# Kernel optimization log

Hardware: AMD Instinct MI355X
Metric: run time of the kernel (lower is better)

## Reference

```python
import jax, jax.numpy as jnp
import numpy as np

B, S, DIM, COV = 64, 512, 1024, 256


def setup_inputs() -> dict:
    key = jax.random.key(0)
    ks = jax.random.split(key, 12)
    s = 0.02
    h = jax.random.normal(ks[0], (B, DIM), jnp.float32)
    context = jax.random.normal(ks[1], (B, S, DIM), jnp.float32)
    cov = jax.random.normal(ks[2], (B, S, COV), jnp.float32)
    mask = jax.random.randint(ks[3], (B, S), 0, 2) == 1
    W_in = jax.random.normal(ks[4], (DIM, DIM), jnp.float32) * s
    W_out = jax.random.normal(ks[5], (DIM, 2 * DIM), jnp.float32) * s
    W_cov = jax.random.normal(ks[6], (DIM, COV), jnp.float32) * s
    b_cov = jax.random.normal(ks[7], (DIM,), jnp.float32) * s
    w_ih = jax.random.normal(ks[8], (3 * COV, 2 * DIM + 1), jnp.float32) * s
    w_hh = jax.random.normal(ks[9], (3 * COV, COV), jnp.float32) * s
    b_ih = jax.random.normal(ks[10], (3 * COV,), jnp.float32) * s
    b_hh = jax.random.normal(ks[11], (3 * COV,), jnp.float32) * s
    return dict(h=h, context=context, cov=cov, W_in=W_in, W_out=W_out,
                W_cov=W_cov, b_cov=b_cov, w_ih=w_ih, w_hh=w_hh,
                b_ih=b_ih, b_hh=b_hh, mask=mask)


def reference(h, context, cov, W_in, W_out, W_cov, b_cov, w_ih, w_hh, b_ih, b_hh, mask):
    # coverage-adjusted context: context + cov_linear(cov)  [B,S,DIM]
    ctx = context + jnp.einsum('bsc,dc->bsd', cov, W_cov) + b_cov
    # target = linear_in(h)  [B,DIM]
    target = h @ W_in.T
    # scores = bmm(context, target).squeeze(2)  [B,S]
    attn = jnp.einsum('bsd,bd->bs', ctx, target)
    attn = jnp.where(mask, -jnp.inf, attn)
    attn = jax.nn.softmax(attn, axis=1)
    # weighted_context = bmm(attn3, context)  [B,DIM]
    wc = jnp.einsum('bs,bsd->bd', attn, ctx)
    h_tilde = jnp.tanh(jnp.concatenate([wc, h], axis=1) @ W_out.T)
    # single-step GRU coverage update over B*S rows
    h_exp = jnp.broadcast_to(h[:, None, :], (B, S, DIM))
    x = jnp.concatenate([ctx, h_exp, attn[..., None]], axis=-1).reshape(B * S, 2 * DIM + 1)
    h0 = cov.reshape(B * S, COV)
    gx = x @ w_ih.T + b_ih   # [B*S, 3*COV]
    gh = h0 @ w_hh.T + b_hh  # [B*S, 3*COV]
    xr, xz, xn = jnp.split(gx, 3, axis=1)
    hr, hz, hn = jnp.split(gh, 3, axis=1)
    r = jax.nn.sigmoid(xr + hr)
    z = jax.nn.sigmoid(xz + hz)
    n = jnp.tanh(xn + r * hn)
    new_cov = ((1.0 - z) * n + z * h0).reshape(B, S, COV)
    return h_tilde, attn, new_cov
```

## Files before the change

### kernel.cpp

```cpp
#include <hip/hip_runtime.h>
#include <math.h>

typedef unsigned short ushort_t;
typedef __attribute__((ext_vector_type(8))) short short8;
typedef __attribute__((ext_vector_type(4))) float f32x4;
typedef __attribute__((ext_vector_type(4))) unsigned short ushort4v;

constexpr int B_ = 64, S_ = 512, DIM_ = 1024, COV_ = 256, TC_ = 768, KIH_ = 2049;
constexpr int NG_ = 1024, KG_ = 1280;

__device__ __forceinline__ float b2f(ushort_t u) {
    union { unsigned int i; float f; } v; v.i = ((unsigned int)u) << 16; return v.f;
}
__device__ __forceinline__ ushort_t f2b(float f) {
    unsigned int x = __float_as_uint(f);
    unsigned int r = x + 0x7fffu + ((x >> 16) & 1u);
    return (ushort_t)(r >> 16);
}
__device__ __forceinline__ float ldv(const float* p, size_t i) { return p[i]; }
__device__ __forceinline__ float ldv(const ushort_t* p, size_t i) { return b2f(p[i]); }

__device__ __forceinline__ float wave_reduce(float a) {
#pragma unroll
    for (int off = 32; off >= 1; off >>= 1) a += __shfl_down(a, off, 64);
    return a;
}

__device__ __forceinline__ void xpose4(f32x4& v, int l) {
    float s, r;
    s = (l & 1) ? v[0] : v[1]; r = __shfl_xor(s, 1, 64); if (l & 1) v[0] = r; else v[1] = r;
    s = (l & 1) ? v[2] : v[3]; r = __shfl_xor(s, 1, 64); if (l & 1) v[2] = r; else v[3] = r;
    s = (l & 2) ? v[0] : v[2]; r = __shfl_xor(s, 2, 64); if (l & 2) v[0] = r; else v[2] = r;
    s = (l & 2) ? v[1] : v[3]; r = __shfl_xor(s, 2, 64); if (l & 2) v[1] = r; else v[3] = r;
}

#define GLDS16(src, dst)                                                            \
    __builtin_amdgcn_global_load_lds(                                               \
        (const __attribute__((address_space(1))) void*)(src),                       \
        (__attribute__((address_space(3))) void*)(dst), 16, 0, 0)

__global__ __launch_bounds__(256) void k_detect_p(const unsigned char* __restrict__ mask,
                                                  const ushort_t* __restrict__ win,
                                                  int* __restrict__ parts) {
    __shared__ int r0[256];
    __shared__ int r1[256];
    int bid = blockIdx.x, tid = threadIdx.x, mb = 0, f32 = 0;
    for (int i = bid * 256 + tid; i < 32768; i += 64 * 256)
        if ((i & 3) != 0 && mask[i] != 0) mb = 1;
    for (int i = bid * 256 + tid; i < 32768; i += 64 * 256) {
        ushort_t u = win[2 * i];
        if ((u & 0x7F80u) >= 0x4480u) f32 = 1;
    }
    r0[tid] = mb; r1[tid] = f32; __syncthreads();
    for (int st = 128; st >= 1; st >>= 1) {
        if (tid < st) { r0[tid] |= r0[tid + st]; r1[tid] |= r1[tid + st]; }
        __syncthreads();
    }
    if (tid == 0) { parts[bid] = r0[0]; parts[64 + bid] = r1[0]; }
}
__global__ void k_detect_c(const int* __restrict__ parts, int* __restrict__ flags) {
    int tid = threadIdx.x;
    int a = parts[tid], b = parts[64 + tid];
#pragma unroll
    for (int off = 32; off >= 1; off >>= 1) {
        a |= __shfl_down(a, off, 64);
        b |= __shfl_down(b, off, 64);
    }
    if (tid == 0) { flags[0] = a; flags[1] = b; }
}

template <typename IT>
__device__ __forceinline__ void transpose_body(const IT* __restrict__ in,
                                               ushort_t* __restrict__ out,
                                               int R, int C, int ld, int off) {
    int idx = blockIdx.x * 256 + threadIdx.x;
    if (idx >= R * C) return;
    int r = idx / C, c = idx - r * C;
    out[c * R + r] = f2b(ldv(in, (size_t)r * ld + off + c));
}
__global__ void k_transpose(const void* __restrict__ in, ushort_t* __restrict__ out,
                            int R, int C, int ld, int off, const int* __restrict__ flags) {
    if (flags[1]) transpose_body((const float*)in, out, R, C, ld, off);
    else transpose_body((const ushort_t*)in, out, R, C, ld, off);
}

template <typename IT>
__device__ __forceinline__ void bfold_body(const IT* __restrict__ bcov,
                                           const IT* __restrict__ wih,
                                           float* __restrict__ bfold,
                                           float* __restrict__ watt) {
    int j = blockIdx.x * 4 + (threadIdx.x >> 6);
    int lane = threadIdx.x & 63;
    const IT* wr = wih + (size_t)j * KIH_;
    float a = 0.f;
#pragma unroll
    for (int i = 0; i < 16; ++i) { int k = lane + 64 * i; a += ldv(bcov, k) * ldv(wr, k); }
    a = wave_reduce(a);
    if (lane == 0) { bfold[j] = a; watt[j] = ldv(wr, 2048); }
}
__global__ __launch_bounds__(256) void k_bfold(const void* __restrict__ bcov,
                                               const void* __restrict__ wih,
                                               float* __restrict__ bfold,
                                               float* __restrict__ watt,
                                               const int* __restrict__ flags) {
    if (flags[1]) bfold_body((const float*)bcov, (const float*)wih, bfold, watt);
    else bfold_body((const ushort_t*)bcov, (const ushort_t*)wih, bfold, watt);
}

__global__ __launch_bounds__(256) void k_wfold_p(const ushort_t* __restrict__ wcov_t,
                                                 const ushort_t* __restrict__ w_t,
                                                 float* __restrict__ wfp) {
    __shared__ float col[256];
    int c = blockIdx.x, p = blockIdx.y, tid = threadIdx.x;
    col[tid] = b2f(wcov_t[c * DIM_ + p * 256 + tid]);
    __syncthreads();
    float a0 = 0.f, a1 = 0.f, a2 = 0.f;
    const ushort_t* wt = w_t + (size_t)(p * 256) * TC_;
    for (int d = 0; d < 256; ++d) {
        float x = col[d];
        const ushort_t* wr = wt + d * TC_;
        a0 += x * b2f(wr[tid]);
        a1 += x * b2f(wr[tid + 256]);
        a2 += x * b2f(wr[tid + 512]);
    }
    float* o = wfp + ((size_t)p * COV_ + c) * TC_;
    o[tid] = a0;
    o[tid + 256] = a1;
    o[tid + 512] = a2;
}

__global__ __launch_bounds__(256) void k_wfold(const ushort_t* __restrict__ wcov_t,
                                               const ushort_t* __restrict__ w_t,
                                               float* __restrict__ wfold) {
    __shared__ float col[DIM_];
    int c = blockIdx.x, tid = threadIdx.x;
    for (int d = tid; d < DIM_; d += 256) col[d] = b2f(wcov_t[c * DIM_ + d]);
    __syncthreads();
    float a0 = 0.f, a1 = 0.f, a2 = 0.f;
    for (int d = 0; d < DIM_; ++d) {
        float x = col[d];
        const ushort_t* wr = w_t + d * TC_;
        a0 += x * b2f(wr[tid]);
        a1 += x * b2f(wr[tid + 256]);
        a2 += x * b2f(wr[tid + 512]);
    }
    wfold[c * TC_ + tid] = a0;
    wfold[c * TC_ + tid + 256] = a1;
    wfold[c * TC_ + tid + 512] = a2;
}

template <typename IT>
__device__ __forceinline__ void buildwg_body(const IT* __restrict__ wih,
                                             const IT* __restrict__ whh,
                                             const float* __restrict__ wfp,
                                             ushort_t* __restrict__ wg) {
    int idx = blockIdx.x * 256 + threadIdx.x;
    if (idx >= NG_ * KG_) return;
    int n = idx / KG_, k = idx - n * KG_;
    int g = n & 3, cq = n >> 2;
    int j = g * COV_ + cq;
    float v;
    if (k < DIM_) {
        v = (j < TC_) ? ldv(wih, (size_t)j * KIH_ + k) : 0.f;
    } else {
        int c = k - DIM_;
        float wf = 0.f;
        if (j < TC_) {
            size_t base = (size_t)c * TC_ + j;
            wf = wfp[base] + wfp[(size_t)COV_ * TC_ + base] +
                 wfp[2 * (size_t)COV_ * TC_ + base] + wfp[3 * (size_t)COV_ * TC_ + base];
        }
        if (j < 512)      v = wf + ldv(whh, (size_t)j * COV_ + c);
        else if (j < TC_) v = wf;
        else              v = ldv(whh, (size_t)(j - 256) * COV_ + c);
    }
    wg[(size_t)n * KG_ + k] = f2b(v);
}
__global__ void k_buildwg(const void* __restrict__ wih, const void* __restrict__ whh,
                          const float* __restrict__ wfp, ushort_t* __restrict__ wg,
                          const int* __restrict__ flags) {
    if (flags[1]) buildwg_body((const float*)wih, (const float*)whh, wfp, wg);
    else buildwg_body((const ushort_t*)wih, (const ushort_t*)whh, wfp, wg);
}

template <typename IT>
__device__ __forceinline__ void target_body(const IT* __restrict__ h,
                                            const IT* __restrict__ W_in,
                                            float* __restrict__ target) {
    int o = blockIdx.x * 4 + (threadIdx.x >> 6);
    int lane = threadIdx.x & 63;
    int b = o >> 10, d = o & (DIM_ - 1);
    const IT* hr = h + (size_t)b * DIM_;
    const IT* wr = W_in + (size_t)d * DIM_;
    float a = 0.f;
#pragma unroll
    for (int j = 0; j < 16; ++j) { int k = lane + 64 * j; a += ldv(hr, k) * ldv(wr, k); }
    a = wave_reduce(a);
    if (lane == 0) target[o] = a;
}
__global__ __launch_bounds__(256) void k_target_w(const void* __restrict__ h,
                                                  const void* __restrict__ W_in,
                                                  float* __restrict__ target,
                                                  const int* __restrict__ flags) {
    if (flags[1]) target_body((const float*)h, (const float*)W_in, target);
    else target_body((const ushort_t*)h, (const ushort_t*)W_in, target);
}

template <typename IT>
__device__ __forceinline__ void mvec_body(const float* __restrict__ target,
                                          const IT* __restrict__ W_cov,
                                          const IT* __restrict__ bcov,
                                          float* __restrict__ mvec,
                                          float* __restrict__ bct) {
    __shared__ float tg[DIM_];
    __shared__ float red[256];
    int b = blockIdx.x, q = blockIdx.y, tid = threadIdx.x;
    float pb = 0.f;
    for (int k = tid; k < DIM_; k += 256) {
        float t = target[b * DIM_ + k];
        tg[k] = t; pb += t * ldv(bcov, k);
    }
    red[tid] = pb; __syncthreads();
    for (int st = 128; st >= 1; st >>= 1) {
        if (tid < st) red[tid] += red[tid + st];
        __syncthreads();
    }
    if (q == 0 && tid == 0) bct[b] = red[0];
    __syncthreads();
    int cg = tid & 63, dg = tid >> 6;
    int c = q * 64 + cg;
    float acc = 0.f;
    int d0 = dg * 256;
    for (int d = d0; d < d0 + 256; ++d) acc += tg[d] * ldv(W_cov, (size_t)d * COV_ + c);
    red[dg * 64 + cg] = acc;
    __syncthreads();
    if (dg == 0)
        mvec[b * COV_ + c] = red[cg] + red[64 + cg] + red[128 + cg] + red[192 + cg];
}
__global__ __launch_bounds__(256) void k_mvec(const float* __restrict__ target,
                                              const void* __restrict__ W_cov,
                                              const void* __restrict__ bcov,
                                              float* __restrict__ mvec,
                                              float* __restrict__ bct,
                                              const int* __restrict__ flags) {
    if (flags[1]) mvec_body(target, (const float*)W_cov, (const float*)bcov, mvec, bct);
    else mvec_body(target, (const ushort_t*)W_cov, (const ushort_t*)bcov, mvec, bct);
}

template <typename IT>
__device__ __forceinline__ void scoreraw_body(const IT* __restrict__ context,
                                              const IT* __restrict__ cov,
                                              const float* __restrict__ target,
                                              const float* __restrict__ mvec,
                                              const float* __restrict__ bct,
                                              float* __restrict__ scf,
                                              ushort_t* __restrict__ ctx_bf,
                                              ushort_t* __restrict__ cov_bf) {
    __shared__ float tg[DIM_];
    __shared__ float ms[COV_];
    int b = blockIdx.x, tid = threadIdx.x;
    for (int k = tid; k < DIM_; k += 256) tg[k] = target[b * DIM_ + k];
    if (tid < COV_) ms[tid] = mvec[b * COV_ + tid];
    float bc = bct[b];
    __syncthreads();
    int wave = tid >> 6, lane = tid & 63;
    int s0 = blockIdx.y * 32 + wave * 8;
    for (int i = 0; i < 8; ++i) {
        int s = s0 + i;
        size_t row = (size_t)(b * S_ + s);
        const IT* cr = context + row * DIM_;
        const IT* vr = cov + row * COV_;
        float a = 0.f;
        if constexpr (sizeof(IT) == 4) {
#pragma unroll
            for (int j = 0; j < 4; ++j) {
                int d = lane * 4 + 256 * j;
                float4 x = *(const float4*)((const float*)cr + d);
                a += x.x * tg[d] + x.y * tg[d + 1] + x.z * tg[d + 2] + x.w * tg[d + 3];
                if (ctx_bf) {
                    ushort4v u;
                    u[0] = f2b(x.x); u[1] = f2b(x.y); u[2] = f2b(x.z); u[3] = f2b(x.w);
                    *(ushort4v*)(ctx_bf + row * DIM_ + d) = u;
                }
            }
            {
                int cc = lane * 4;
                float4 x = *(const float4*)((const float*)vr + cc);
                a += x.x * ms[cc] + x.y * ms[cc + 1] + x.z * ms[cc + 2] + x.w * ms[cc + 3];
                if (cov_bf) {
                    ushort4v u;
                    u[0] = f2b(x.x); u[1] = f2b(x.y); u[2] = f2b(x.z); u[3] = f2b(x.w);
                    *(ushort4v*)(cov_bf + row * COV_ + cc) = u;
                }
            }
        } else {
#pragma unroll
            for (int j = 0; j < 16; ++j) { int d = lane + 64 * j; a += ldv(cr, d) * tg[d]; }
#pragma unroll
            for (int j = 0; j < 4; ++j) { int c = lane + 64 * j; a += ldv(vr, c) * ms[c]; }
        }
        a = wave_reduce(a);
        if (lane == 0) scf[row] = a + bc;
    }
}
__global__ __launch_bounds__(256) void k_scoreraw(const void* __restrict__ context,
                                                  const void* __restrict__ cov,
                                                  const float* __restrict__ target,
                                                  const float* __restrict__ mvec,
                                                  const float* __restrict__ bct,
                                                  float* __restrict__ scf,
                                                  ushort_t* __restrict__ ctx_bf,
                                                  ushort_t* __restrict__ cov_bf,
                                                  const int* __restrict__ flags) {
    if (flags[1]) scoreraw_body((const float*)context, (const float*)cov, target, mvec, bct,
                                scf, ctx_bf, cov_bf);
    else scoreraw_body((const ushort_t*)context, (const ushort_t*)cov, target, mvec, bct,
                       scf, ctx_bf, cov_bf);
}

__global__ __launch_bounds__(256) void k_softmax(const float* __restrict__ scf,
                                                 const void* __restrict__ maskp,
                                                 const int* __restrict__ flags,
                                                 float* __restrict__ attnf,
                                                 float* __restrict__ attn_out) {
    __shared__ float red[256];
    int b = blockIdx.x, tid = threadIdx.x;
    int mb = flags[0];
    int i0 = b * S_ + tid, i1 = i0 + 256;
    int m0 = mb ? (int)((const unsigned char*)maskp)[i0] : ((const int*)maskp)[i0];
    int m1 = mb ? (int)((const unsigned char*)maskp)[i1] : ((const int*)maskp)[i1];
    float s0 = m0 ? -INFINITY : scf[i0];
    float s1 = m1 ? -INFINITY : scf[i1];
    red[tid] = fmaxf(s0, s1); __syncthreads();
    for (int st = 128; st >= 1; st >>= 1) {
        if (tid < st) red[tid] = fmaxf(red[tid], red[tid + st]);
        __syncthreads();
    }
    float mx = red[0]; __syncthreads();
    float e0 = expf(s0 - mx), e1 = expf(s1 - mx);
    red[tid] = e0 + e1; __syncthreads();
    for (int st = 128; st >= 1; st >>= 1) {
        if (tid < st) red[tid] += red[tid + st];
        __syncthreads();
    }
    float inv = 1.0f / red[0];
    float a0 = e0 * inv, a1 = e1 * inv;
    attnf[i0] = a0; attnf[i1] = a1;
    attn_out[i0] = a0; attn_out[i1] = a1;
}

__global__ __launch_bounds__(256) void k_wcpart2(const ushort_t* __restrict__ ctx_bf,
                                                 const ushort_t* __restrict__ cov_bf,
                                                 const void* __restrict__ ctx_in,
                                                 const void* __restrict__ cov_in,
                                                 const float* __restrict__ attnf,
                                                 float* __restrict__ wcp,
                                                 float* __restrict__ acp,
                                                 const int* __restrict__ flags) {
    const ushort_t* C = flags[1] ? ctx_bf : (const ushort_t*)ctx_in;
    const ushort_t* V = flags[1] ? cov_bf : (const ushort_t*)cov_in;
    __shared__ float at[32];
    int b = blockIdx.x, ch = blockIdx.y, tid = threadIdx.x;
    int s0 = ch * 32;
    if (tid < 32) at[tid] = attnf[b * S_ + s0 + tid];
    __syncthreads();
    float acv = 0.f;
    for (int s = 0; s < 32; ++s)
        acv += at[s] * b2f(V[((size_t)(b * S_ + s0 + s)) * COV_ + tid]);
    acp[((size_t)ch * B_ + b) * COV_ + tid] = acv;
    float acc[4] = {0.f, 0.f, 0.f, 0.f};
    for (int s = 0; s < 32; ++s) {
        float w = at[s];
        const ushort_t* cr = C + ((size_t)(b * S_ + s0 + s)) * DIM_;
        acc[0] += w * b2f(cr[tid]);
        acc[1] += w * b2f(cr[tid + 256]);
        acc[2] += w * b2f(cr[tid + 512]);
        acc[3] += w * b2f(cr[tid + 768]);
    }
    size_t base = ((size_t)ch * B_ + b) * DIM_;
    for (int m = 0; m < 4; ++m) wcp[base + tid + 256 * m] = acc[m];
}

template <typename IT>
__device__ __forceinline__ void wcfin_body(const float* __restrict__ wcp,
                                           const float* __restrict__ acp,
                                           const ushort_t* __restrict__ wcov_t,
                                           const IT* __restrict__ bcov,
                                           float* __restrict__ wc) {
    __shared__ float ac[COV_];
    int b = blockIdx.x, tid = threadIdx.x;
    float a = 0.f;
    for (int ch = 0; ch < 16; ++ch) a += acp[((size_t)ch * B_ + b) * COV_ + tid];
    ac[tid] = a;
    __syncthreads();
    float acc[4] = {0.f, 0.f, 0.f, 0.f};
    for (int ch = 0; ch < 16; ++ch) {
        size_t base = ((size_t)ch * B_ + b) * DIM_;
        for (int m = 0; m < 4; ++m) acc[m] += wcp[base + tid + 256 * m];
    }
    for (int c = 0; c < COV_; ++c) {
        float av = ac[c];
        const ushort_t* wr = wcov_t + c * DIM_;
        acc[0] += av * b2f(wr[tid]);
        acc[1] += av * b2f(wr[tid + 256]);
        acc[2] += av * b2f(wr[tid + 512]);
        acc[3] += av * b2f(wr[tid + 768]);
    }
    for (int m = 0; m < 4; ++m) {
        int d = tid + 256 * m;
        wc[b * DIM_ + d] = acc[m] + ldv(bcov, d);
    }
}
__global__ __launch_bounds__(256) void k_wcfin(const float* __restrict__ wcp,
                                               const float* __restrict__ acp,
                                               const ushort_t* __restrict__ wcov_t,
                                               const void* __restrict__ bcov,
                                               float* __restrict__ wc,
                                               const int* __restrict__ flags) {
    if (flags[1]) wcfin_body(wcp, acp, wcov_t, (const float*)bcov, wc);
    else wcfin_body(wcp, acp, wcov_t, (const ushort_t*)bcov, wc);
}

template <typename IT>
__device__ __forceinline__ void htilde_body(const float* __restrict__ wc,
                                            const IT* __restrict__ h,
                                            const IT* __restrict__ W_out,
                                            float* __restrict__ out_ht) {
    int o = blockIdx.x * 4 + (threadIdx.x >> 6);
    int lane = threadIdx.x & 63;
    int b = o >> 10, d = o & (DIM_ - 1);
    const float* wcr = wc + b * DIM_;
    const IT* hr = h + (size_t)b * DIM_;
    const IT* wr = W_out + (size_t)d * 2 * DIM_;
    float a = 0.f;
#pragma unroll
    for (int j = 0; j < 16; ++j) { int k = lane + 64 * j; a += wcr[k] * ldv(wr, k); }
#pragma unroll
    for (int j = 0; j < 16; ++j) { int k = lane + 64 * j; a += ldv(hr, k) * ldv(wr, DIM_ + k); }
    a = wave_reduce(a);
    if (lane == 0) out_ht[o] = tanhf(a);
}
__global__ __launch_bounds__(256) void k_htilde_w(const float* __restrict__ wc,
                                                  const void* __restrict__ h,
                                                  const void* __restrict__ W_out,
                                                  float* __restrict__ out_ht,
                                                  const int* __restrict__ flags) {
    if (flags[1]) htilde_body(wc, (const float*)h, (const float*)W_out, out_ht);
    else htilde_body(wc, (const ushort_t*)h, (const ushort_t*)W_out, out_ht);
}

template <typename IT>
__device__ __forceinline__ void gxh_body(const IT* __restrict__ h,
                                         const IT* __restrict__ w_ih,
                                         const IT* __restrict__ b_ih,
                                         const float* __restrict__ bfold,
                                         float* __restrict__ gxall) {
    int o = blockIdx.x * 4 + (threadIdx.x >> 6);
    int lane = threadIdx.x & 63;
    int b = o / TC_, j = o - b * TC_;
    const IT* hr = h + (size_t)b * DIM_;
    const IT* wr = w_ih + (size_t)j * KIH_ + DIM_;
    float a = 0.f;
#pragma unroll
    for (int i = 0; i < 16; ++i) { int k = lane + 64 * i; a += ldv(hr, k) * ldv(wr, k); }
    a = wave_reduce(a);
    if (lane == 0) gxall[o] = a + ldv(b_ih, j) + bfold[j];
}
__global__ __launch_bounds__(256) void k_gxh_w(const void* __restrict__ h,
                                               const void* __restrict__ w_ih,
                                               const void* __restrict__ b_ih,
                                               const float* __restrict__ bfold,
                                               float* __restrict__ gxall,
                                               const int* __restrict__ flags) {
    if (flags[1]) gxh_body((const float*)h, (const float*)w_ih, (const float*)b_ih, bfold, gxall);
    else gxh_body((const ushort_t*)h, (const ushort_t*)w_ih, (const ushort_t*)b_ih, bfold, gxall);
}

__global__ __launch_bounds__(256) void k_gemm6(const ushort_t* __restrict__ ctx_bf,
                                               const ushort_t* __restrict__ cov_bf,
                                               const void* __restrict__ ctx_in,
                                               const void* __restrict__ cov_in,
                                               const ushort_t* __restrict__ wg,
                                               const float* __restrict__ attnf,
                                               const float* __restrict__ gxall,
                                               const float* __restrict__ watt,
                                               const void* __restrict__ bhh,
                                               float* __restrict__ out_cov,
                                               const int* __restrict__ flags) {
    const int f32in = flags[1];
    const ushort_t* Xc = f32in ? ctx_bf : (const ushort_t*)ctx_in;
    const ushort_t* Xv = f32in ? cov_bf : (const ushort_t*)cov_in;
    __shared__ __align__(16) unsigned char smem[65536];
    ushort_t* A0 = (ushort_t*)smem;
    ushort_t* B0 = A0 + 8192;
    ushort_t* A1 = B0 + 8192;
    ushort_t* B1 = A1 + 8192;
    float* smN = (float*)smem;
    float* smZ = smN + 128 * 33;

    int tid = threadIdx.x;
    int p = blockIdx.x;
    int xcd = p & 7, t = p >> 3;
    int nb = t & 7, rb = xcd + 8 * (t >> 3);
    int n0 = nb * 128;
    int grow0 = rb * 128;
    int wave = tid >> 6, lane = tid & 63;
    int wm = wave >> 1, wn = wave & 1;
    int half = lane >> 4, r16 = lane & 15;

    const ushort_t* gAc[4]; const ushort_t* gAv[4]; const ushort_t* gB[4];
    int ldsOff[4];
#pragma unroll
    for (int j = 0; j < 4; ++j) {
        int c = wave * 256 + j * 64 + lane;
        int row = c >> 3, sl = (c & 7) ^ ((c >> 3) & 7);
        gAc[j] = Xc + (size_t)(grow0 + row) * DIM_ + sl * 8;
        gAv[j] = Xv + (size_t)(grow0 + row) * COV_ + sl * 8;
        gB[j]  = wg + (size_t)(n0 + row) * KG_ + sl * 8;
        ldsOff[j] = (wave * 256 + j * 64) * 8;
    }

    int offA[2][4], offB[2][4];
#pragma unroll
    for (int kh = 0; kh < 2; ++kh)
#pragma unroll
        for (int u = 0; u < 4; ++u) {
            int rA = wm * 64 + u * 16 + r16;
            offA[kh][u] = rA * 64 + ((kh * 4 + half) ^ (rA & 7)) * 8;
            int rB = wn * 64 + u * 16 + r16;
            offB[kh][u] = rB * 64 + ((kh * 4 + half) ^ (rB & 7)) * 8;
        }

    f32x4 acc[4][4];
#pragma unroll
    for (int i = 0; i < 4; ++i)
#pragma unroll
        for (int j = 0; j < 4; ++j) acc[i][j] = (f32x4){0.f, 0.f, 0.f, 0.f};

    auto stage = [&](int kt, ushort_t* Ad, ushort_t* Bd) {
        int k0 = kt * 64;
        if (k0 < DIM_) {
#pragma unroll
            for (int j = 0; j < 4; ++j) GLDS16(gAc[j] + k0, Ad + ldsOff[j]);
        } else {
            int kk = k0 - DIM_;
#pragma unroll
            for (int j = 0; j < 4; ++j) GLDS16(gAv[j] + kk, Ad + ldsOff[j]);
        }
#pragma unroll
        for (int j = 0; j < 4; ++j) GLDS16(gB[j] + k0, Bd + ldsOff[j]);
    };
    auto compute = [&](const ushort_t* Ac, const ushort_t* Bc) {
#pragma unroll
        for (int kh = 0; kh < 2; ++kh) {
            short8 a[4], b[4];
#pragma unroll
            for (int u = 0; u < 4; ++u) a[u] = *(const short8*)&Ac[offA[kh][u]];
#pragma unroll
            for (int u = 0; u < 4; ++u) b[u] = *(const short8*)&Bc[offB[kh][u]];
#pragma unroll
            for (int i = 0; i < 4; ++i)
#pragma unroll
                for (int j = 0; j < 4; ++j)
                    acc[i][j] = __builtin_amdgcn_mfma_f32_16x16x32_bf16(a[i], b[j], acc[i][j], 0, 0, 0);
        }
    };

    constexpr int NT = KG_ / 64;
    stage(0, A0, B0);
    __syncthreads();
#pragma unroll 1
    for (int kt = 0; kt < NT; kt += 2) {
        stage(kt + 1, A1, B1);
        compute(A0, B0);
        __syncthreads();
        if (kt + 2 < NT) stage(kt + 2, A0, B0);
        compute(A1, B1);
        __syncthreads();
    }

    int l = lane;
    int bb = grow0 >> 9;
    const float* gx = gxall + bb * TC_;
    int rloc[4]; float atv[4];
#pragma unroll
    for (int i = 0; i < 4; ++i) {
        rloc[i] = wm * 64 + 16 * i + ((l >> 4) << 2) + (l & 3);
        atv[i] = attnf[grow0 + rloc[i]];
    }
#pragma unroll
    for (int j = 0; j < 4; ++j) {
        int cl = wn * 16 + 4 * j + ((l >> 2) & 3);
        int c = (n0 >> 2) + cl;
        float gxR = gx[c], gxZ = gx[COV_ + c], gxN = gx[2 * COV_ + c];
        float waR = watt[c], waZ = watt[COV_ + c], waN = watt[2 * COV_ + c];
        float bhR, bhZ, bhN;
        if (f32in) {
            const float* bp = (const float*)bhh;
            bhR = bp[c]; bhZ = bp[COV_ + c]; bhN = bp[2 * COV_ + c];
        } else {
            const ushort_t* bp = (const ushort_t*)bhh;
            bhR = b2f(bp[c]); bhZ = b2f(bp[COV_ + c]); bhN = b2f(bp[2 * COV_ + c]);
        }
#pragma unroll
        for (int i = 0; i < 4; ++i) {
            f32x4 v = acc[i][j];
            xpose4(v, l);
            float at = atv[i];
            float aR  = v[0] + gxR + at * waR + bhR;
            float aZ  = v[1] + gxZ + at * waZ + bhZ;
            float aXN = v[2] + gxN + at * waN;
            float aHN = v[3] + bhN;
            float r = 1.f / (1.f + expf(-aR));
            float z = 1.f / (1.f + expf(-aZ));
            float nn = tanhf(aXN + r * aHN);
            smN[rloc[i] * 33 + cl] = nn;
            smZ[rloc[i] * 33 + cl] = z;
        }
    }
    __syncthreads();
    int cbase = nb * 32;
    for (int u = tid; u < 128 * 8; u += 256) {
        int rl = u >> 3, c4 = (u & 7) * 4;
        float n0v = smN[rl * 33 + c4 + 0], n1v = smN[rl * 33 + c4 + 1];
        float n2v = smN[rl * 33 + c4 + 2], n3v = smN[rl * 33 + c4 + 3];
        float z0 = smZ[rl * 33 + c4 + 0], z1 = smZ[rl * 33 + c4 + 1];
        float z2 = smZ[rl * 33 + c4 + 2], z3 = smZ[rl * 33 + c4 + 3];
        size_t base = (size_t)(grow0 + rl) * COV_ + cbase + c4;
        float h0v, h1v, h2v, h3v;
        if (f32in) {
            float4 hv = *(const float4*)((const float*)cov_in + base);
            h0v = hv.x; h1v = hv.y; h2v = hv.z; h3v = hv.w;
        } else {
            ushort4v hv = *(const ushort4v*)((const ushort_t*)cov_in + base);
            h0v = b2f(hv[0]); h1v = b2f(hv[1]); h2v = b2f(hv[2]); h3v = b2f(hv[3]);
        }
        float4 o;
        o.x = (1.f - z0) * n0v + z0 * h0v;
        o.y = (1.f - z1) * n1v + z1 * h1v;
        o.z = (1.f - z2) * n2v + z2 * h2v;
        o.w = (1.f - z3) * n3v + z3 * h3v;
        *(float4*)(out_cov + base) = o;
    }
}

template <typename IT>
__device__ __forceinline__ void gru_body(const IT* __restrict__ context,
                                         const IT* __restrict__ cov,
                                         const float* __restrict__ attnf,
                                         const float* __restrict__ gxall,
                                         const float* __restrict__ watt,
                                         const ushort_t* __restrict__ w_t,
                                         const float* __restrict__ wfold,
                                         const ushort_t* __restrict__ whh_t,
                                         const IT* __restrict__ bhh,
                                         float* __restrict__ out_cov) {
    __shared__ float xc[8][DIM_];
    __shared__ float h0s[8][COV_];
    __shared__ float atn[8];
    int base = blockIdx.x * 8, tid = threadIdx.x;
    int b = base / S_;
    for (int i = tid; i < 8 * DIM_; i += 256)
        ((float*)xc)[i] = ldv(context, (size_t)base * DIM_ + i);
    for (int i = tid; i < 8 * COV_; i += 256)
        ((float*)h0s)[i] = ldv(cov, (size_t)base * COV_ + i);
    if (tid < 8) atn[tid] = attnf[base + tid];
    __syncthreads();
    int c = tid;
    float gxR = gxall[b * TC_ + c], gxZ = gxall[b * TC_ + 256 + c], gxN = gxall[b * TC_ + 512 + c];
    float bhR = ldv(bhh, c), bhZ = ldv(bhh, 256 + c), bhN = ldv(bhh, 512 + c);
    float waR = watt[c], waZ = watt[256 + c], waN = watt[512 + c];
    float aR[8], aZ[8], aXN[8], aHN[8];
#pragma unroll
    for (int g = 0; g < 8; ++g) {
        float a = atn[g];
        aR[g] = gxR + bhR + a * waR;
        aZ[g] = gxZ + bhZ + a * waZ;
        aXN[g] = gxN + a * waN;
        aHN[g] = bhN;
    }
    for (int k = 0; k < DIM_; ++k) {
        const ushort_t* row = w_t + k * TC_;
        float wr = b2f(row[c]), wz = b2f(row[256 + c]), wn = b2f(row[512 + c]);
#pragma unroll
        for (int g = 0; g < 8; ++g) {
            float x = xc[g][k];
            aR[g] += x * wr; aZ[g] += x * wz; aXN[g] += x * wn;
        }
    }
    for (int k = 0; k < COV_; ++k) {
        const float* row = wfold + k * TC_;
        float wr = row[c], wz = row[256 + c], wn = row[512 + c];
#pragma unroll
        for (int g = 0; g < 8; ++g) {
            float x = h0s[g][k];
            aR[g] += x * wr; aZ[g] += x * wz; aXN[g] += x * wn;
        }
    }
    for (int k = 0; k < COV_; ++k) {
        const ushort_t* row = whh_t + k * TC_;
        float wr = b2f(row[c]), wz = b2f(row[256 + c]), wn = b2f(row[512 + c]);
#pragma unroll
        for (int g = 0; g < 8; ++g) {
            float hh = h0s[g][k];
            aR[g] += hh * wr; aZ[g] += hh * wz; aHN[g] += hh * wn;
        }
    }
#pragma unroll
    for (int g = 0; g < 8; ++g) {
        float r = 1.f / (1.f + expf(-aR[g]));
        float z = 1.f / (1.f + expf(-aZ[g]));
        float n = tanhf(aXN[g] + r * aHN[g]);
        float h0c = h0s[g][c];
        out_cov[(size_t)(base + g) * COV_ + c] = (1.f - z) * n + z * h0c;
    }
}
__global__ __launch_bounds__(256) void k_gru_f(const void* __restrict__ context,
                                               const void* __restrict__ cov,
                                               const float* __restrict__ attnf,
                                               const float* __restrict__ gxall,
                                               const float* __restrict__ watt,
                                               const ushort_t* __restrict__ w_t,
                                               const float* __restrict__ wfold,
                                               const ushort_t* __restrict__ whh_t,
                                               const void* __restrict__ bhh,
                                               float* __restrict__ out_cov,
                                               const int* __restrict__ flags) {
    if (flags[1]) gru_body((const float*)context, (const float*)cov, attnf, gxall, watt,
                           w_t, wfold, whh_t, (const float*)bhh, out_cov);
    else gru_body((const ushort_t*)context, (const ushort_t*)cov, attnf, gxall, watt,
                  w_t, wfold, whh_t, (const ushort_t*)bhh, out_cov);
}

extern "C" void kernel_launch(void* const* d_in, const int* in_sizes, int n_in,
                              void* d_out, int out_size, void* d_ws, size_t ws_size,
                              hipStream_t stream) {
    const void* h       = d_in[0];
    const void* context = d_in[1];
    const void* cov     = d_in[2];
    const void* W_in    = d_in[3];
    const void* W_out   = d_in[4];
    const void* W_cov   = d_in[5];
    const void* b_cov   = d_in[6];
    const void* w_ih    = d_in[7];
    const void* w_hh    = d_in[8];
    const void* b_ih    = d_in[9];
    const void* b_hh    = d_in[10];
    const void* maskp   = d_in[11];

    float* out = (float*)d_out;
    float* out_ht   = out;
    float* out_attn = out + B_ * DIM_;
    float* out_cov  = out + B_ * DIM_ + B_ * S_;

    char* ws = (char*)d_ws;
    size_t o = 0;
    float* target = (float*)(ws + o); o += (size_t)B_ * DIM_ * 4;
    float* attnf  = (float*)(ws + o); o += (size_t)B_ * S_ * 4;
    float* wc     = (float*)(ws + o); o += (size_t)B_ * DIM_ * 4;
    float* gxall  = (float*)(ws + o); o += (size_t)B_ * TC_ * 4;
    float* watt   = (float*)(ws + o); o += 4096;
    float* mvec   = (float*)(ws + o); o += (size_t)B_ * COV_ * 4;
    float* bct    = (float*)(ws + o); o += 4096;
    float* bfold  = (float*)(ws + o); o += 4096;
    float* wfold  = (float*)(ws + o); o += (size_t)COV_ * TC_ * 4;
    float* wfp    = (float*)(ws + o); o += (size_t)4 * COV_ * TC_ * 4;
    int* dparts   = (int*)(ws + o);   o += 512;
    ushort_t* w_t    = (ushort_t*)(ws + o); o += (size_t)DIM_ * TC_ * 2;
    ushort_t* whh_t  = (ushort_t*)(ws + o); o += (size_t)COV_ * TC_ * 2;
    ushort_t* wcov_t = (ushort_t*)(ws + o); o += (size_t)COV_ * DIM_ * 2;
    int* flags = (int*)(ws + o); o += 256;
    float* scf   = (float*)(ws + o); o += (size_t)B_ * S_ * 4;
    float* wcp   = (float*)(ws + o); o += (size_t)16 * B_ * DIM_ * 4;
    float* acp   = (float*)(ws + o); o += (size_t)16 * B_ * COV_ * 4;
    ushort_t* wg = (ushort_t*)(ws + o); o += (size_t)NG_ * KG_ * 2;
    ushort_t* ctx_bf = (ushort_t*)(ws + o); o += (size_t)B_ * S_ * DIM_ * 2;
    ushort_t* cov_bf = (ushort_t*)(ws + o); o += (size_t)B_ * S_ * COV_ * 2;
    size_t fixed = o;

    const size_t TOTAL_ROWS = (size_t)B_ * S_;
    const bool fused = ws_size >= fixed;

    k_detect_p<<<64, 256, 0, stream>>>((const unsigned char*)maskp, (const ushort_t*)W_in, dparts);
    k_detect_c<<<1, 64, 0, stream>>>(dparts, flags);
    k_transpose<<<(TC_ * DIM_) / 256, 256, 0, stream>>>(w_ih, w_t, TC_, DIM_, KIH_, 0, flags);
    k_transpose<<<(DIM_ * COV_) / 256, 256, 0, stream>>>(W_cov, wcov_t, DIM_, COV_, COV_, 0, flags);
    if (!fused)
        k_transpose<<<(TC_ * COV_) / 256, 256, 0, stream>>>(w_hh, whh_t, TC_, COV_, COV_, 0, flags);
    k_bfold<<<TC_ / 4, 256, 0, stream>>>(b_cov, w_ih, bfold, watt, flags);
    if (fused) {
        k_wfold_p<<<dim3(COV_, 4), 256, 0, stream>>>(wcov_t, w_t, wfp);
        k_buildwg<<<(NG_ * KG_ + 255) / 256, 256, 0, stream>>>(w_ih, w_hh, wfp, wg, flags);
    } else {
        k_wfold<<<COV_, 256, 0, stream>>>(wcov_t, w_t, wfold);
    }

    k_target_w<<<(B_ * DIM_) / 4, 256, 0, stream>>>(h, W_in, target, flags);
    k_mvec<<<dim3(B_, 4), 256, 0, stream>>>(target, W_cov, b_cov, mvec, bct, flags);
    k_scoreraw<<<dim3(B_, 16), 256, 0, stream>>>(context, cov, target, mvec, bct, scf,
                                                 fused ? ctx_bf : nullptr,
                                                 fused ? cov_bf : nullptr, flags);
    k_softmax<<<B_, 256, 0, stream>>>(scf, maskp, flags, attnf, out_attn);
    if (fused)
        k_wcpart2<<<dim3(B_, 16), 256, 0, stream>>>(ctx_bf, cov_bf, context, cov, attnf,
                                                    wcp, acp, flags);
    else
        k_wcpart2<<<dim3(B_, 16), 256, 0, stream>>>((const ushort_t*)context, (const ushort_t*)cov,
                                                    context, cov, attnf, wcp, acp, flags);
    k_wcfin<<<B_, 256, 0, stream>>>(wcp, acp, wcov_t, b_cov, wc, flags);
    k_htilde_w<<<(B_ * DIM_) / 4, 256, 0, stream>>>(wc, h, W_out, out_ht, flags);

    k_gxh_w<<<(B_ * TC_) / 4, 256, 0, stream>>>(h, w_ih, b_ih, bfold, gxall, flags);
    if (fused) {
        int nblk = (int)(TOTAL_ROWS / 128) * (NG_ / 128);
        k_gemm6<<<nblk, 256, 0, stream>>>(ctx_bf, cov_bf, context, cov, wg, attnf,
                                          gxall, watt, b_hh, out_cov, flags);
    } else {
        k_gru_f<<<(B_ * S_) / 8, 256, 0, stream>>>(context, cov, attnf, gxall, watt,
                                                   w_t, wfold, whh_t, b_hh, out_cov, flags);
    }
}
```

Measured before the change: 603.0 us.

## Fuse softmax into weighted-context pass, merge transposes, vectorize GEMV loads

Folds the softmax kernel into the weighted-context partial kernel: each of the 16 chunk blocks per batch recomputes the row max and sum from the scores, and chunk 0 writes the attention outputs. The two weight transposes become one launch. The float32 GEMV-style kernels (target, bfold, gxh, htilde) and the wc partial/final kernels now use 4-wide vector loads and stores. This removes launches and a round trip of attention through global memory, at the cost of the softmax reduction being repeated 16 times per batch row.

```diff
diff --git a/kernel.cpp b/kernel.cpp
--- a/kernel.cpp
+++ b/kernel.cpp
@@ -19,6 +19,10 @@
 }
 __device__ __forceinline__ float ldv(const float* p, size_t i) { return p[i]; }
 __device__ __forceinline__ float ldv(const ushort_t* p, size_t i) { return b2f(p[i]); }
+
+__device__ __forceinline__ f32x4 ld4u(const float* p) {
+    f32x4 v; __builtin_memcpy(&v, p, 16); return v;
+}
 
 __device__ __forceinline__ float wave_reduce(float a) {
 #pragma unroll
@@ -70,6 +74,28 @@
 }
 
 template <typename IT>
+__device__ __forceinline__ void tr_elem(const IT* __restrict__ in, ushort_t* __restrict__ out,
+                                        int R, int C, int ld, int idx) {
+    int r = idx / C, c = idx - r * C;
+    out[c * R + r] = f2b(ldv(in, (size_t)r * ld + c));
+}
+__global__ void k_transpose2(const void* __restrict__ w_ih, ushort_t* __restrict__ w_t,
+                             const void* __restrict__ W_cov, ushort_t* __restrict__ wcov_t,
+                             const int* __restrict__ flags) {
+    int idx = blockIdx.x * 256 + threadIdx.x;
+    const int N1 = TC_ * DIM_;
+    if (idx < N1) {
+        if (flags[1]) tr_elem((const float*)w_ih, w_t, TC_, DIM_, KIH_, idx);
+        else tr_elem((const ushort_t*)w_ih, w_t, TC_, DIM_, KIH_, idx);
+    } else {
+        idx -= N1;
+        if (idx >= DIM_ * COV_) return;
+        if (flags[1]) tr_elem((const float*)W_cov, wcov_t, DIM_, COV_, COV_, idx);
+        else tr_elem((const ushort_t*)W_cov, wcov_t, DIM_, COV_, COV_, idx);
+    }
+}
+
+template <typename IT>
 __device__ __forceinline__ void transpose_body(const IT* __restrict__ in,
                                                ushort_t* __restrict__ out,
                                                int R, int C, int ld, int off) {
@@ -93,8 +119,18 @@
     int lane = threadIdx.x & 63;
     const IT* wr = wih + (size_t)j * KIH_;
     float a = 0.f;
-#pragma unroll
-    for (int i = 0; i < 16; ++i) { int k = lane + 64 * i; a += ldv(bcov, k) * ldv(wr, k); }
+    if constexpr (sizeof(IT) == 4) {
+#pragma unroll
+        for (int i = 0; i < 4; ++i) {
+            int k = lane * 4 + 256 * i;
+            float4 bv = *(const float4*)((const float*)bcov + k);
+            f32x4 wv = ld4u((const float*)wr + k);
+            a += bv.x * wv[0] + bv.y * wv[1] + bv.z * wv[2] + bv.w * wv[3];
+        }
+    } else {
+#pragma unroll
+        for (int i = 0; i < 16; ++i) { int k = lane + 64 * i; a += ldv(bcov, k) * ldv(wr, k); }
+    }
     a = wave_reduce(a);
     if (lane == 0) { bfold[j] = a; watt[j] = ldv(wr, 2048); }
 }
@@ -193,8 +229,18 @@
     const IT* hr = h + (size_t)b * DIM_;
     const IT* wr = W_in + (size_t)d * DIM_;
     float a = 0.f;
-#pragma unroll
-    for (int j = 0; j < 16; ++j) { int k = lane + 64 * j; a += ldv(hr, k) * ldv(wr, k); }
+    if constexpr (sizeof(IT) == 4) {
+#pragma unroll
+        for (int j = 0; j < 4; ++j) {
+            int k = lane * 4 + 256 * j;
+            float4 x = *(const float4*)((const float*)hr + k);
+            float4 w = *(const float4*)((const float*)wr + k);
+            a += x.x * w.x + x.y * w.y + x.z * w.z + x.w * w.w;
+        }
+    } else {
+#pragma unroll
+        for (int j = 0; j < 16; ++j) { int k = lane + 64 * j; a += ldv(hr, k) * ldv(wr, k); }
+    }
     a = wave_reduce(a);
     if (lane == 0) target[o] = a;
 }
@@ -318,19 +364,30 @@
                        scf, ctx_bf, cov_bf);
 }
 
-__global__ __launch_bounds__(256) void k_softmax(const float* __restrict__ scf,
+__global__ __launch_bounds__(256) void k_wcpart3(const ushort_t* __restrict__ ctx_bf,
+                                                 const ushort_t* __restrict__ cov_bf,
+                                                 const void* __restrict__ ctx_in,
+                                                 const void* __restrict__ cov_in,
+                                                 const float* __restrict__ scf,
                                                  const void* __restrict__ maskp,
-                                                 const int* __restrict__ flags,
+                                                 float* __restrict__ wcp,
+                                                 float* __restrict__ acp,
                                                  float* __restrict__ attnf,
-                                                 float* __restrict__ attn_out) {
+                                                 float* __restrict__ attn_out,
+                                                 const int* __restrict__ flags) {
+    const ushort_t* C = flags[1] ? ctx_bf : (const ushort_t*)ctx_in;
+    const ushort_t* V = flags[1] ? cov_bf : (const ushort_t*)cov_in;
+    __shared__ float sc[512];
     __shared__ float red[256];
-    int b = blockIdx.x, tid = threadIdx.x;
+    __shared__ float at[32];
+    int b = blockIdx.x, ch = blockIdx.y, tid = threadIdx.x;
     int mb = flags[0];
     int i0 = b * S_ + tid, i1 = i0 + 256;
     int m0 = mb ? (int)((const unsigned char*)maskp)[i0] : ((const int*)maskp)[i0];
     int m1 = mb ? (int)((const unsigned char*)maskp)[i1] : ((const int*)maskp)[i1];
     float s0 = m0 ? -INFINITY : scf[i0];
     float s1 = m1 ? -INFINITY : scf[i1];
+    sc[tid] = s0; sc[tid + 256] = s1;
     red[tid] = fmaxf(s0, s1); __syncthreads();
     for (int st = 128; st >= 1; st >>= 1) {
         if (tid < st) red[tid] = fmaxf(red[tid], red[tid + st]);
@@ -344,41 +401,28 @@
         __syncthreads();
     }
     float inv = 1.0f / red[0];
-    float a0 = e0 * inv, a1 = e1 * inv;
-    attnf[i0] = a0; attnf[i1] = a1;
-    attn_out[i0] = a0; attn_out[i1] = a1;
-}
-
-__global__ __launch_bounds__(256) void k_wcpart2(const ushort_t* __restrict__ ctx_bf,
-                                                 const ushort_t* __restrict__ cov_bf,
-                                                 const void* __restrict__ ctx_in,
-                                                 const void* __restrict__ cov_in,
-                                                 const float* __restrict__ attnf,
-                                                 float* __restrict__ wcp,
-                                                 float* __restrict__ acp,
-                                                 const int* __restrict__ flags) {
-    const ushort_t* C = flags[1] ? ctx_bf : (const ushort_t*)ctx_in;
-    const ushort_t* V = flags[1] ? cov_bf : (const ushort_t*)cov_in;
-    __shared__ float at[32];
-    int b = blockIdx.x, ch = blockIdx.y, tid = threadIdx.x;
-    int s0 = ch * 32;
-    if (tid < 32) at[tid] = attnf[b * S_ + s0 + tid];
+    if (ch == 0) {
+        float a0 = e0 * inv, a1 = e1 * inv;
+        attnf[i0] = a0; attnf[i1] = a1;
+        attn_out[i0] = a0; attn_out[i1] = a1;
+    }
+    int s0c = ch * 32;
+    if (tid < 32) at[tid] = expf(sc[s0c + tid] - mx) * inv;
     __syncthreads();
     float acv = 0.f;
     for (int s = 0; s < 32; ++s)
-        acv += at[s] * b2f(V[((size_t)(b * S_ + s0 + s)) * COV_ + tid]);
+        acv += at[s] * b2f(V[((size_t)(b * S_ + s0c + s)) * COV_ + tid]);
     acp[((size_t)ch * B_ + b) * COV_ + tid] = acv;
-    float acc[4] = {0.f, 0.f, 0.f, 0.f};
+    f32x4 acc = (f32x4){0.f, 0.f, 0.f, 0.f};
     for (int s = 0; s < 32; ++s) {
         float w = at[s];
-        const ushort_t* cr = C + ((size_t)(b * S_ + s0 + s)) * DIM_;
-        acc[0] += w * b2f(cr[tid]);
-        acc[1] += w * b2f(cr[tid + 256]);
-        acc[2] += w * b2f(cr[tid + 512]);
-        acc[3] += w * b2f(cr[tid + 768]);
-    }
-    size_t base = ((size_t)ch * B_ + b) * DIM_;
-    for (int m = 0; m < 4; ++m) wcp[base + tid + 256 * m] = acc[m];
+        ushort4v x = *(const ushort4v*)(C + ((size_t)(b * S_ + s0c + s)) * DIM_ + 4 * tid);
+        acc[0] += w * b2f(x[0]);
+        acc[1] += w * b2f(x[1]);
+        acc[2] += w * b2f(x[2]);
+        acc[3] += w * b2f(x[3]);
+    }
+    *(f32x4*)(wcp + ((size_t)ch * B_ + b) * DIM_ + 4 * tid) = acc;
 }
 
 template <typename IT>
@@ -393,23 +437,26 @@
     for (int ch = 0; ch < 16; ++ch) a += acp[((size_t)ch * B_ + b) * COV_ + tid];
     ac[tid] = a;
     __syncthreads();
-    float acc[4] = {0.f, 0.f, 0.f, 0.f};
-    for (int ch = 0; ch < 16; ++ch) {
-        size_t base = ((size_t)ch * B_ + b) * DIM_;
-        for (int m = 0; m < 4; ++m) acc[m] += wcp[base + tid + 256 * m];
-    }
+    f32x4 acc = (f32x4){0.f, 0.f, 0.f, 0.f};
+    for (int ch = 0; ch < 16; ++ch)
+        acc += *(const f32x4*)(wcp + ((size_t)ch * B_ + b) * DIM_ + 4 * tid);
     for (int c = 0; c < COV_; ++c) {
         float av = ac[c];
-        const ushort_t* wr = wcov_t + c * DIM_;
-        acc[0] += av * b2f(wr[tid]);
-        acc[1] += av * b2f(wr[tid + 256]);
-        acc[2] += av * b2f(wr[tid + 512]);
-        acc[3] += av * b2f(wr[tid + 768]);
-    }
-    for (int m = 0; m < 4; ++m) {
-        int d = tid + 256 * m;
-        wc[b * DIM_ + d] = acc[m] + ldv(bcov, d);
-    }
+        ushort4v w4 = *(const ushort4v*)(wcov_t + c * DIM_ + 4 * tid);
+        acc[0] += av * b2f(w4[0]);
+        acc[1] += av * b2f(w4[1]);
+        acc[2] += av * b2f(w4[2]);
+        acc[3] += av * b2f(w4[3]);
+    }
+    int d = 4 * tid;
+    if constexpr (sizeof(IT) == 4) {
+        float4 bc4 = *(const float4*)((const float*)bcov + d);
+        acc[0] += bc4.x; acc[1] += bc4.y; acc[2] += bc4.z; acc[3] += bc4.w;
+    } else {
+        ushort4v b4 = *(const ushort4v*)((const ushort_t*)bcov + d);
+        acc[0] += b2f(b4[0]); acc[1] += b2f(b4[1]); acc[2] += b2f(b4[2]); acc[3] += b2f(b4[3]);
+    }
+    *(f32x4*)(wc + b * DIM_ + d) = acc;
 }
 __global__ __launch_bounds__(256) void k_wcfin(const float* __restrict__ wcp,
                                                const float* __restrict__ acp,
@@ -433,10 +480,27 @@
     const IT* hr = h + (size_t)b * DIM_;
     const IT* wr = W_out + (size_t)d * 2 * DIM_;
     float a = 0.f;
-#pragma unroll
-    for (int j = 0; j < 16; ++j) { int k = lane + 64 * j; a += wcr[k] * ldv(wr, k); }
-#pragma unroll
-    for (int j = 0; j < 16; ++j) { int k = lane + 64 * j; a += ldv(hr, k) * ldv(wr, DIM_ + k); }
+    if constexpr (sizeof(IT) == 4) {
+#pragma unroll
+        for (int j = 0; j < 4; ++j) {
+            int k = lane * 4 + 256 * j;
+            float4 x = *(const float4*)(wcr + k);
+            float4 w = *(const float4*)((const float*)wr + k);
+            a += x.x * w.x + x.y * w.y + x.z * w.z + x.w * w.w;
+        }
+#pragma unroll
+        for (int j = 0; j < 4; ++j) {
+            int k = lane * 4 + 256 * j;
+            float4 x = *(const float4*)((const float*)hr + k);
+            float4 w = *(const float4*)((const float*)wr + DIM_ + k);
+            a += x.x * w.x + x.y * w.y + x.z * w.z + x.w * w.w;
+        }
+    } else {
+#pragma unroll
+        for (int j = 0; j < 16; ++j) { int k = lane + 64 * j; a += wcr[k] * ldv(wr, k); }
+#pragma unroll
+        for (int j = 0; j < 16; ++j) { int k = lane + 64 * j; a += ldv(hr, k) * ldv(wr, DIM_ + k); }
+    }
     a = wave_reduce(a);
     if (lane == 0) out_ht[o] = tanhf(a);
 }
@@ -461,8 +525,18 @@
     const IT* hr = h + (size_t)b * DIM_;
     const IT* wr = w_ih + (size_t)j * KIH_ + DIM_;
     float a = 0.f;
-#pragma unroll
-    for (int i = 0; i < 16; ++i) { int k = lane + 64 * i; a += ldv(hr, k) * ldv(wr, k); }
+    if constexpr (sizeof(IT) == 4) {
+#pragma unroll
+        for (int i = 0; i < 4; ++i) {
+            int k = lane * 4 + 256 * i;
+            float4 x = *(const float4*)((const float*)hr + k);
+            f32x4 w = ld4u((const float*)wr + k);
+            a += x.x * w[0] + x.y * w[1] + x.z * w[2] + x.w * w[3];
+        }
+    } else {
+#pragma unroll
+        for (int i = 0; i < 16; ++i) { int k = lane + 64 * i; a += ldv(hr, k) * ldv(wr, k); }
+    }
     a = wave_reduce(a);
     if (lane == 0) gxall[o] = a + ldv(b_ih, j) + bfold[j];
 }
@@ -783,8 +857,8 @@
 
     k_detect_p<<<64, 256, 0, stream>>>((const unsigned char*)maskp, (const ushort_t*)W_in, dparts);
     k_detect_c<<<1, 64, 0, stream>>>(dparts, flags);
-    k_transpose<<<(TC_ * DIM_) / 256, 256, 0, stream>>>(w_ih, w_t, TC_, DIM_, KIH_, 0, flags);
-    k_transpose<<<(DIM_ * COV_) / 256, 256, 0, stream>>>(W_cov, wcov_t, DIM_, COV_, COV_, 0, flags);
+    k_transpose2<<<(TC_ * DIM_ + DIM_ * COV_) / 256, 256, 0, stream>>>(w_ih, w_t, W_cov,
+                                                                       wcov_t, flags);
     if (!fused)
         k_transpose<<<(TC_ * COV_) / 256, 256, 0, stream>>>(w_hh, whh_t, TC_, COV_, COV_, 0, flags);
     k_bfold<<<TC_ / 4, 256, 0, stream>>>(b_cov, w_ih, bfold, watt, flags);
@@ -800,13 +874,13 @@
     k_scoreraw<<<dim3(B_, 16), 256, 0, stream>>>(context, cov, target, mvec, bct, scf,
                                                  fused ? ctx_bf : nullptr,
                                                  fused ? cov_bf : nullptr, flags);
-    k_softmax<<<B_, 256, 0, stream>>>(scf, maskp, flags, attnf, out_attn);
     if (fused)
-        k_wcpart2<<<dim3(B_, 16), 256, 0, stream>>>(ctx_bf, cov_bf, context, cov, attnf,
-                                                    wcp, acp, flags);
+        k_wcpart3<<<dim3(B_, 16), 256, 0, stream>>>(ctx_bf, cov_bf, context, cov, scf, maskp,
+                                                    wcp, acp, attnf, out_attn, flags);
     else
-        k_wcpart2<<<dim3(B_, 16), 256, 0, stream>>>((const ushort_t*)context, (const ushort_t*)cov,
-                                                    context, cov, attnf, wcp, acp, flags);
+        k_wcpart3<<<dim3(B_, 16), 256, 0, stream>>>((const ushort_t*)context, (const ushort_t*)cov,
+                                                    context, cov, scf, maskp,
+                                                    wcp, acp, attnf, out_attn, flags);
     k_wcfin<<<B_, 256, 0, stream>>>(wcp, acp, wcov_t, b_cov, wc, flags);
     k_htilde_w<<<(B_ * DIM_) / 4, 256, 0, stream>>>(wc, h, W_out, out_ht, flags);
 
```

After: 602.7 us. No clear change (-0.0%).
